# Performance work log

Measured on AMD Instinct MI355X. Metric: run time of the kernel, lower is better.

## Reference

```python
import jax, jax.numpy as jnp
import numpy as np

N = 100000
E = 1600000
IN_C, HID_C, OUT_C = 128, 128, 64


def setup_inputs() -> dict:
    key = jax.random.key(0)
    k_x, k_e, k_w1, k_w2 = jax.random.split(key, 4)
    x = jax.random.normal(k_x, (N, IN_C), dtype=jnp.float32)
    edge_index = jax.random.randint(k_e, (2, E), 0, N, dtype=jnp.int32)
    # nn.Linear default init: U(-1/sqrt(fan_in), 1/sqrt(fan_in)); bias init zeros per module
    lim1 = 1.0 / np.sqrt(IN_C)
    lim2 = 1.0 / np.sqrt(HID_C)
    W1 = jax.random.uniform(k_w1, (IN_C, HID_C), minval=-lim1, maxval=lim1, dtype=jnp.float32)
    b1 = jnp.zeros((HID_C,), dtype=jnp.float32)
    W2 = jax.random.uniform(k_w2, (HID_C, OUT_C), minval=-lim2, maxval=lim2, dtype=jnp.float32)
    b2 = jnp.zeros((OUT_C,), dtype=jnp.float32)
    return {"x": x, "edge_index": edge_index, "W1": W1, "b1": b1, "W2": W2, "b2": b2}


def _out_degree_gcn_conv(x, src, dst, W, b, n_nodes):
    # linear projection (no bias in lin)
    h = x @ W  # [N, out_c]
    # out-degree of each source node
    deg = jax.ops.segment_sum(jnp.ones((src.shape[0],), dtype=h.dtype), src, num_segments=n_nodes)
    deg_inv = 1.0 / jnp.maximum(deg, 1.0)  # clamp(min=1)
    h = h * deg_inv[:, None]
    # message: x_j = h[src]; aggregate: sum at dst
    out = jax.ops.segment_sum(h[src], dst, num_segments=n_nodes)  # [N, out_c]
    return out + b


def reference(x, edge_index, W1, b1, W2, b2):
    src, dst = edge_index[0], edge_index[1]
    n = x.shape[0]
    h = _out_degree_gcn_conv(x, src, dst, W1, b1, n)
    h = jax.nn.relu(h)
    # dropout p=0.0 -> identity
    out = _out_degree_gcn_conv(h, src, dst, W2, b2, n)
    return out
```

## Files before the change

### kernel.cpp

```cpp
#include <hip/hip_runtime.h>
#include <hip/hip_bf16.h>


typedef __attribute__((ext_vector_type(8))) short short8;
typedef __attribute__((ext_vector_type(4))) float floatx4;

__device__ inline unsigned short f2bf(float f) {
    union { float f; unsigned u; } v; v.f = f;
    return (unsigned short)((v.u + 0x8000u) >> 16);
}
__device__ inline float bf2f(unsigned b) {
    union { unsigned u; float f; } v; v.u = b << 16;
    return v.f;
}
__device__ inline float bf2f_hi(unsigned b) {
    union { unsigned u; float f; } v; v.u = b & 0xFFFF0000u;
    return v.f;
}

#define NBMAX 512
#define CAP   8192
#define CHUNK 8192

__global__ __launch_bounds__(256) void convw_kernel(
    const float* __restrict__ W1, const float* __restrict__ W2,
    unsigned short* __restrict__ Wb1, unsigned short* __restrict__ Wb2,
    int* __restrict__ cnt)
{
    int i = blockIdx.x * 256 + threadIdx.x;
    if (i < NBMAX * 32) cnt[i] = 0;
    if (i < 128 * 128) {
        int k = i >> 7, n = i & 127;
        Wb1[n * 128 + k] = f2bf(W1[k * 128 + n]);
    }
    i -= 128 * 128;
    if (i >= 0 && i < 128 * 64) {
        int k = i >> 6, n = i & 63;
        Wb2[n * 128 + k] = f2bf(W2[k * 64 + n]);
    }
}

#define SCAN512(lb, t)                                    \
    for (int o = 1; o < 512; o <<= 1) {                   \
        int add_ = ((t) >= o) ? lb[(t) - o] : 0;          \
        __syncthreads();                                  \
        lb[t] += add_;                                    \
        __syncthreads();                                  \
    }

__global__ __launch_bounds__(512) void scatter2_kernel(
    const int* __restrict__ src, const int* __restrict__ dst, int E,
    int* __restrict__ cnt_d, int* __restrict__ cnt_s,
    unsigned* __restrict__ pairs, unsigned char* __restrict__ srcs_b, int NB,
    const float* __restrict__ x, unsigned short* __restrict__ xb, int NF8)
{
    const int EB = (E + CHUNK - 1) / CHUNK;
    if ((int)blockIdx.x >= EB) {
        int i = ((int)blockIdx.x - EB) * 512 + threadIdx.x;
        if (i < NF8) {
            float4 a0 = ((const float4*)x)[(size_t)i * 2];
            float4 a1 = ((const float4*)x)[(size_t)i * 2 + 1];
            uint4 st;
            st.x = (unsigned)f2bf(a0.x) | ((unsigned)f2bf(a0.y) << 16);
            st.y = (unsigned)f2bf(a0.z) | ((unsigned)f2bf(a0.w) << 16);
            st.z = (unsigned)f2bf(a1.x) | ((unsigned)f2bf(a1.y) << 16);
            st.w = (unsigned)f2bf(a1.z) | ((unsigned)f2bf(a1.w) << 16);
            ((uint4*)xb)[i] = st;
        }
        return;
    }
    __shared__ int hd[NBMAX], lb[512], bd[NBMAX], cd_[NBMAX];
    __shared__ unsigned staged[CHUNK];
    const int t = threadIdx.x;
    const int e0 = blockIdx.x * CHUNK;
    const int e1 = min(e0 + CHUNK, E);
    const int cnt = e1 - e0;

    for (int i = t; i < NB; i += 512) { hd[i] = 0; cd_[i] = 0; }
    __syncthreads();
    for (int i = e0 + t; i < e1; i += 512)
        atomicAdd(&hd[dst[i] >> 8], 1);
    __syncthreads();
    lb[t] = (t < NB) ? hd[t] : 0;
    __syncthreads();
    SCAN512(lb, t)
    for (int i = t; i < NB; i += 512)
        if (hd[i]) bd[i] = atomicAdd(&cnt_d[i * 16], hd[i]);
    __syncthreads();
    for (int i = e0 + t; i < e1; i += 512) {
        int sv = src[i], dv = dst[i];
        int b = dv >> 8;
        int slot = atomicAdd(&cd_[b], 1);
        staged[lb[b] - hd[b] + slot] = ((unsigned)(dv & 255) << 24) | (unsigned)sv;
    }
    __syncthreads();
    for (int i = t; i < cnt; i += 512) {
        int lo = 0, hi = NB - 1;
        while (lo < hi) { int mid = (lo + hi) >> 1; if (lb[mid] > i) hi = mid; else lo = mid + 1; }
        int b = lo;
        pairs[(size_t)b * CAP + bd[b] + (i - (lb[b] - hd[b]))] = staged[i];
    }
    __syncthreads();

    unsigned char* stb = (unsigned char*)staged;
    for (int i = t; i < NB; i += 512) { hd[i] = 0; cd_[i] = 0; }
    __syncthreads();
    for (int i = e0 + t; i < e1; i += 512)
        atomicAdd(&hd[src[i] >> 8], 1);
    __syncthreads();
    lb[t] = (t < NB) ? hd[t] : 0;
    __syncthreads();
    SCAN512(lb, t)
    for (int i = t; i < NB; i += 512)
        if (hd[i]) bd[i] = atomicAdd(&cnt_s[i * 16], hd[i]);
    __syncthreads();
    for (int i = e0 + t; i < e1; i += 512) {
        int sv = src[i];
        int b = sv >> 8;
        int slot = atomicAdd(&cd_[b], 1);
        stb[lb[b] - hd[b] + slot] = (unsigned char)(sv & 255);
    }
    __syncthreads();
    for (int i = t; i < cnt; i += 512) {
        int lo = 0, hi = NB - 1;
        while (lo < hi) { int mid = (lo + hi) >> 1; if (lb[mid] > i) hi = mid; else lo = mid + 1; }
        int b = lo;
        srcs_b[(size_t)b * CAP + bd[b] + (i - (lb[b] - hd[b]))] = stb[i];
    }
}

__global__ __launch_bounds__(256) void bucket_finalize_kernel(
    const unsigned* __restrict__ pairs, const unsigned char* __restrict__ srcs_b,
    const int* __restrict__ cnt_d, const int* __restrict__ cnt_s,
    int* __restrict__ sorted_src, int2* __restrict__ se,
    float* __restrict__ deg_inv, int N)
{
    const int b = blockIdx.x;
    const int node0 = b << 8;
    const int t = threadIdx.x;
    const size_t base = (size_t)b * CAP;
    __shared__ int hist[256];
    __shared__ int cur[256];
    __shared__ int pre[256];

    const int cd = cnt_d[b * 16];
    hist[t] = 0;
    __syncthreads();
    for (int i = t; i < cd; i += 256)
        atomicAdd(&hist[pairs[base + i] >> 24], 1);
    __syncthreads();
    int v = hist[t];
    int v4 = (v + 3) & ~3;
    pre[t] = v4;
    __syncthreads();
    for (int o = 1; o < 256; o <<= 1) {
        int add = (t >= o) ? pre[t - o] : 0;
        __syncthreads();
        pre[t] += add;
        __syncthreads();
    }
    int excl = pre[t] - v4;
    cur[t] = excl;
    if (node0 + t < N) {
        se[node0 + t] = make_int2((int)base + excl, (int)base + excl + v);
        for (int i = v; i < v4; ++i) sorted_src[base + excl + i] = N;
    }
    __syncthreads();
    for (int i = t; i < cd; i += 256) {
        unsigned p = pairs[base + i];
        int pos = atomicAdd(&cur[p >> 24], 1);
        sorted_src[base + pos] = (int)(p & 0xFFFFFFu);
    }

    __syncthreads();
    hist[t] = 0;
    __syncthreads();
    const int cs = cnt_s[b * 16];
    for (int i = t; i < cs; i += 256)
        atomicAdd(&hist[srcs_b[base + i]], 1);
    __syncthreads();
    if (node0 + t < N) {
        int d = hist[t];
        deg_inv[node0 + t] = 1.0f / (float)(d < 1 ? 1 : d);
    }
}

template <int NC, int SC>
__global__ __launch_bounds__(256) void gemm_mfma_kernel(
    const unsigned short* __restrict__ Ab, const unsigned short* __restrict__ Wb,
    const float* __restrict__ scale, unsigned short* __restrict__ Cb, int M)
{
    constexpr int NT = NC / 16;
    const int t = threadIdx.x;
    if (blockIdx.x == 0 && t < NC / 2)
        ((unsigned*)Cb)[(size_t)M * (NC / 2) + t] = 0;
    const int wm = t >> 6;
    const int lane = t & 63;
    const int lm = lane & 15;
    const int lk = (lane >> 4) * 8;

    const int r0 = blockIdx.x * 64 + wm * 16;
    int row = r0 + lm;
    if (row >= M) row = M - 1;

    floatx4 acc[NT];
#pragma unroll
    for (int j = 0; j < NT; ++j) acc[j] = (floatx4){0.f, 0.f, 0.f, 0.f};

#pragma unroll
    for (int kk = 0; kk < 4; ++kk) {
        const int kb = kk * 32 + lk;
        short8 af = *(const short8*)&Ab[(size_t)row * 128 + kb];
#pragma unroll
        for (int j = 0; j < NT; ++j) {
            short8 bfr = *(const short8*)&Wb[(size_t)(j * 16 + lm) * 128 + kb];
            acc[j] = __builtin_amdgcn_mfma_f32_16x16x32_bf16(af, bfr, acc[j], 0, 0, 0);
        }
    }

    const int rbase = r0 + (lane >> 4) * 4;
#pragma unroll
    for (int reg = 0; reg < 4; ++reg) {
        int rg = rbase + reg;
        if (rg < M) {
            float di = SC ? scale[rg] : 1.0f;
#pragma unroll
            for (int j = 0; j < NT; ++j)
                Cb[(size_t)rg * NC + j * 16 + lm] = f2bf(SC ? acc[j][reg] * di : acc[j][reg]);
        }
    }
}

#define LD128(vv, ii) uint2 vv = *(const uint2*)&val[(size_t)(ii) * 64 + 2 * l]
#define ACC8_128(I0, I1) do { \
    LD128(v0, I0.x); LD128(v1, I0.y); LD128(v2, I0.z); LD128(v3, I0.w); \
    LD128(v4, I1.x); LD128(v5, I1.y); LD128(v6, I1.z); LD128(v7, I1.w); \
    a0 += ((bf2f(v0.x & 0xFFFF) + bf2f(v1.x & 0xFFFF)) + (bf2f(v2.x & 0xFFFF) + bf2f(v3.x & 0xFFFF))) \
        + ((bf2f(v4.x & 0xFFFF) + bf2f(v5.x & 0xFFFF)) + (bf2f(v6.x & 0xFFFF) + bf2f(v7.x & 0xFFFF))); \
    a1 += ((bf2f_hi(v0.x) + bf2f_hi(v1.x)) + (bf2f_hi(v2.x) + bf2f_hi(v3.x))) \
        + ((bf2f_hi(v4.x) + bf2f_hi(v5.x)) + (bf2f_hi(v6.x) + bf2f_hi(v7.x))); \
    a2 += ((bf2f(v0.y & 0xFFFF) + bf2f(v1.y & 0xFFFF)) + (bf2f(v2.y & 0xFFFF) + bf2f(v3.y & 0xFFFF))) \
        + ((bf2f(v4.y & 0xFFFF) + bf2f(v5.y & 0xFFFF)) + (bf2f(v6.y & 0xFFFF) + bf2f(v7.y & 0xFFFF))); \
    a3 += ((bf2f_hi(v0.y) + bf2f_hi(v1.y)) + (bf2f_hi(v2.y) + bf2f_hi(v3.y))) \
        + ((bf2f_hi(v4.y) + bf2f_hi(v5.y)) + (bf2f_hi(v6.y) + bf2f_hi(v7.y))); \
} while (0)
#define ACC4_128(I0) do { \
    LD128(v0, I0.x); LD128(v1, I0.y); LD128(v2, I0.z); LD128(v3, I0.w); \
    a0 += (bf2f(v0.x & 0xFFFF) + bf2f(v1.x & 0xFFFF)) + (bf2f(v2.x & 0xFFFF) + bf2f(v3.x & 0xFFFF)); \
    a1 += (bf2f_hi(v0.x) + bf2f_hi(v1.x)) + (bf2f_hi(v2.x) + bf2f_hi(v3.x)); \
    a2 += (bf2f(v0.y & 0xFFFF) + bf2f(v1.y & 0xFFFF)) + (bf2f(v2.y & 0xFFFF) + bf2f(v3.y & 0xFFFF)); \
    a3 += (bf2f_hi(v0.y) + bf2f_hi(v1.y)) + (bf2f_hi(v2.y) + bf2f_hi(v3.y)); \
} while (0)

__global__ __launch_bounds__(256) void aggregate128_kernel(
    const int2* __restrict__ se, const int* __restrict__ sorted_src,
    const unsigned* __restrict__ val, const float* __restrict__ bias,
    const float* __restrict__ deg_inv, unsigned* __restrict__ outb, int N)
{
    int node = blockIdx.x * 8 + (threadIdx.x >> 5);
    if (node >= N) return;
    int l = threadIdx.x & 31;
    int2 r = se[node];
    int e = r.x;
    const int end4 = r.x + ((r.y - r.x + 3) & ~3);
    float a0 = 0.f, a1 = 0.f, a2 = 0.f, a3 = 0.f;

    if (e + 8 <= end4) {
        int4 i0 = *(const int4*)&sorted_src[e];
        int4 i1 = *(const int4*)&sorted_src[e + 4];
        for (; e + 16 <= end4; e += 8) {
            int4 n0 = *(const int4*)&sorted_src[e + 8];
            int4 n1 = *(const int4*)&sorted_src[e + 12];
            ACC8_128(i0, i1);
            i0 = n0; i1 = n1;
        }
        ACC8_128(i0, i1);
        e += 8;
    }
    if (e < end4) {
        int4 i0 = *(const int4*)&sorted_src[e];
        ACC4_128(i0);
    }

    float di = deg_inv[node];
    float4 bv = *(const float4*)&bias[4 * l];
    a0 = fmaxf(a0 + bv.x, 0.f) * di;
    a1 = fmaxf(a1 + bv.y, 0.f) * di;
    a2 = fmaxf(a2 + bv.z, 0.f) * di;
    a3 = fmaxf(a3 + bv.w, 0.f) * di;
    uint2 o;
    o.x = (unsigned)f2bf(a0) | ((unsigned)f2bf(a1) << 16);
    o.y = (unsigned)f2bf(a2) | ((unsigned)f2bf(a3) << 16);
    *(uint2*)&outb[(size_t)node * 64 + 2 * l] = o;
}

#define LD64(vv, ii) unsigned vv = val[(size_t)(ii) * 32 + l]
#define ACC8_64(I0, I1) do { \
    LD64(v0, I0.x); LD64(v1, I0.y); LD64(v2, I0.z); LD64(v3, I0.w); \
    LD64(v4, I1.x); LD64(v5, I1.y); LD64(v6, I1.z); LD64(v7, I1.w); \
    ax += ((bf2f(v0 & 0xFFFF) + bf2f(v1 & 0xFFFF)) + (bf2f(v2 & 0xFFFF) + bf2f(v3 & 0xFFFF))) \
        + ((bf2f(v4 & 0xFFFF) + bf2f(v5 & 0xFFFF)) + (bf2f(v6 & 0xFFFF) + bf2f(v7 & 0xFFFF))); \
    ay += ((bf2f_hi(v0) + bf2f_hi(v1)) + (bf2f_hi(v2) + bf2f_hi(v3))) \
        + ((bf2f_hi(v4) + bf2f_hi(v5)) + (bf2f_hi(v6) + bf2f_hi(v7))); \
} while (0)
#define ACC4_64(I0) do { \
    LD64(v0, I0.x); LD64(v1, I0.y); LD64(v2, I0.z); LD64(v3, I0.w); \
    ax += (bf2f(v0 & 0xFFFF) + bf2f(v1 & 0xFFFF)) + (bf2f(v2 & 0xFFFF) + bf2f(v3 & 0xFFFF)); \
    ay += (bf2f_hi(v0) + bf2f_hi(v1)) + (bf2f_hi(v2) + bf2f_hi(v3)); \
} while (0)

__global__ __launch_bounds__(256) void aggregate64_kernel(
    const int2* __restrict__ se, const int* __restrict__ sorted_src,
    const unsigned* __restrict__ val, const float* __restrict__ bias,
    float* __restrict__ out, int N)
{
    int node = blockIdx.x * 8 + (threadIdx.x >> 5);
    if (node >= N) return;
    int l = threadIdx.x & 31;
    int2 r = se[node];
    int e = r.x;
    const int end4 = r.x + ((r.y - r.x + 3) & ~3);
    float ax = 0.f, ay = 0.f;

    if (e + 8 <= end4) {
        int4 i0 = *(const int4*)&sorted_src[e];
        int4 i1 = *(const int4*)&sorted_src[e + 4];
        for (; e + 16 <= end4; e += 8) {
            int4 n0 = *(const int4*)&sorted_src[e + 8];
            int4 n1 = *(const int4*)&sorted_src[e + 12];
            ACC8_64(i0, i1);
            i0 = n0; i1 = n1;
        }
        ACC8_64(i0, i1);
        e += 8;
    }
    if (e < end4) {
        int4 i0 = *(const int4*)&sorted_src[e];
        ACC4_64(i0);
    }

    float2 o = make_float2(ax + bias[2 * l], ay + bias[2 * l + 1]);
    *(float2*)&out[(size_t)node * 64 + 2 * l] = o;
}

extern "C" void kernel_launch(void* const* d_in, const int* in_sizes, int n_in,
                              void* d_out, int out_size, void* d_ws, size_t ws_size,
                              hipStream_t stream) {
    const float* x  = (const float*)d_in[0];
    const int*   ei = (const int*)d_in[1];
    const float* W1 = (const float*)d_in[2];
    const float* b1 = (const float*)d_in[3];
    const float* W2 = (const float*)d_in[4];
    const float* b2 = (const float*)d_in[5];
    float* out = (float*)d_out;

    const int N = in_sizes[0] / 128;
    const int E = in_sizes[1] / 2;
    const int* src = ei;
    const int* dst = ei + E;
    const int NB = (N + 255) >> 8;

    char* ws = (char*)d_ws;
    size_t off = 0;
    auto alloc = [&](size_t bytes) {
        void* p = ws + off;
        off = (off + bytes + 255) & ~(size_t)255;
        return p;
    };
    float* deg_inv  = (float*)alloc((size_t)N * 4);
    int2*  se       = (int2*)alloc((size_t)N * 8);
    int*   cnt_d    = (int*)alloc((size_t)NBMAX * 16 * 4 * 2);
    int*   cnt_s    = cnt_d + (size_t)NBMAX * 16;
    unsigned short* Wb1 = (unsigned short*)alloc((size_t)128 * 128 * 2);
    unsigned short* Wb2 = (unsigned short*)alloc((size_t)64 * 128 * 2);
    unsigned*      pairs  = (unsigned*)alloc((size_t)NBMAX * CAP * 4);
    unsigned char* srcs_b = (unsigned char*)alloc((size_t)NBMAX * CAP);
    int*   sorted_src = (int*)alloc((size_t)NBMAX * CAP * 4);
    unsigned short* h    = (unsigned short*)alloc((size_t)(N + 1) * 128 * 2);
    unsigned short* out1 = (unsigned short*)alloc((size_t)N * 128 * 2);
    unsigned short* xb = out1;
    unsigned short* g = ((size_t)(N + 1) * 128 <= (size_t)NBMAX * CAP * 4)
                            ? (unsigned short*)pairs
                            : (unsigned short*)alloc((size_t)(N + 1) * 64 * 2);

    convw_kernel<<<96, 256, 0, stream>>>(W1, W2, Wb1, Wb2, cnt_d);

    const int EB = (E + CHUNK - 1) / CHUNK;
    const int NF8 = (N * 128) / 8;
    const int CB = (NF8 + 511) / 512;
    scatter2_kernel<<<EB + CB, 512, 0, stream>>>(src, dst, E, cnt_d, cnt_s,
                                                 pairs, srcs_b, NB, x, xb, NF8);
    bucket_finalize_kernel<<<NB, 256, 0, stream>>>(pairs, srcs_b, cnt_d, cnt_s,
                                                   sorted_src, se, deg_inv, N);

    const int gblocks = (N + 63) / 64;
    const int ablocks = (N + 7) / 8;
    gemm_mfma_kernel<128, 1><<<gblocks, 256, 0, stream>>>(xb, Wb1, deg_inv, h, N);
    aggregate128_kernel<<<ablocks, 256, 0, stream>>>(se, sorted_src, (const unsigned*)h, b1,
                                                     deg_inv, (unsigned*)out1, N);
    gemm_mfma_kernel<64, 0><<<gblocks, 256, 0, stream>>>(out1, Wb2, nullptr, g, N);
    aggregate64_kernel<<<ablocks, 256, 0, stream>>>(se, sorted_src, (const unsigned*)g, b2, out, N);
}
```

Measured before the change: 306.8 us.

## Split scatter into per-key blocks, widen blocks, use warp-per-bucket copyout

The scatter kernel now launches separate blocks for the dst-bucketing and src-bucketing phases instead of running both sequentially in one block, and block size goes from 512 to 1024 threads. The per-element binary search for the global copyout is replaced by one wavefront per bucket copying contiguous runs. bucket_finalize goes from 256 to 512 threads. The aim is more parallelism and cheaper, coalesced writes in the preprocessing stage, at the cost of more blocks, more barriers and heavier per-block LDS use.

```diff
diff --git a/kernel.cpp b/kernel.cpp
--- a/kernel.cpp
+++ b/kernel.cpp
@@ -40,23 +40,17 @@
     }
 }
 
-#define SCAN512(lb, t)                                    \
-    for (int o = 1; o < 512; o <<= 1) {                   \
-        int add_ = ((t) >= o) ? lb[(t) - o] : 0;          \
-        __syncthreads();                                  \
-        lb[t] += add_;                                    \
-        __syncthreads();                                  \
-    }
-
-__global__ __launch_bounds__(512) void scatter2_kernel(
+__global__ __launch_bounds__(1024) void scatter2_kernel(
     const int* __restrict__ src, const int* __restrict__ dst, int E,
     int* __restrict__ cnt_d, int* __restrict__ cnt_s,
     unsigned* __restrict__ pairs, unsigned char* __restrict__ srcs_b, int NB,
     const float* __restrict__ x, unsigned short* __restrict__ xb, int NF8)
 {
     const int EB = (E + CHUNK - 1) / CHUNK;
-    if ((int)blockIdx.x >= EB) {
-        int i = ((int)blockIdx.x - EB) * 512 + threadIdx.x;
+    const int t = threadIdx.x;
+    const int bid = blockIdx.x;
+    if (bid >= 2 * EB) {
+        int i = (bid - 2 * EB) * 1024 + t;
         if (i < NF8) {
             float4 a0 = ((const float4*)x)[(size_t)i * 2];
             float4 a1 = ((const float4*)x)[(size_t)i * 2 + 1];
@@ -69,67 +63,70 @@
         }
         return;
     }
-    __shared__ int hd[NBMAX], lb[512], bd[NBMAX], cd_[NBMAX];
+    __shared__ int hd[NBMAX], lb[NBMAX], bd[NBMAX], cd_[NBMAX];
     __shared__ unsigned staged[CHUNK];
-    const int t = threadIdx.x;
-    const int e0 = blockIdx.x * CHUNK;
+    const bool phaseA = (bid < EB);
+    const int c = phaseA ? bid : bid - EB;
+    const int e0 = c * CHUNK;
     const int e1 = min(e0 + CHUNK, E);
-    const int cnt = e1 - e0;
-
-    for (int i = t; i < NB; i += 512) { hd[i] = 0; cd_[i] = 0; }
-    __syncthreads();
-    for (int i = e0 + t; i < e1; i += 512)
-        atomicAdd(&hd[dst[i] >> 8], 1);
-    __syncthreads();
-    lb[t] = (t < NB) ? hd[t] : 0;
-    __syncthreads();
-    SCAN512(lb, t)
-    for (int i = t; i < NB; i += 512)
-        if (hd[i]) bd[i] = atomicAdd(&cnt_d[i * 16], hd[i]);
-    __syncthreads();
-    for (int i = e0 + t; i < e1; i += 512) {
-        int sv = src[i], dv = dst[i];
-        int b = dv >> 8;
-        int slot = atomicAdd(&cd_[b], 1);
-        staged[lb[b] - hd[b] + slot] = ((unsigned)(dv & 255) << 24) | (unsigned)sv;
-    }
-    __syncthreads();
-    for (int i = t; i < cnt; i += 512) {
-        int lo = 0, hi = NB - 1;
-        while (lo < hi) { int mid = (lo + hi) >> 1; if (lb[mid] > i) hi = mid; else lo = mid + 1; }
-        int b = lo;
-        pairs[(size_t)b * CAP + bd[b] + (i - (lb[b] - hd[b]))] = staged[i];
-    }
-    __syncthreads();
-
-    unsigned char* stb = (unsigned char*)staged;
-    for (int i = t; i < NB; i += 512) { hd[i] = 0; cd_[i] = 0; }
-    __syncthreads();
-    for (int i = e0 + t; i < e1; i += 512)
-        atomicAdd(&hd[src[i] >> 8], 1);
-    __syncthreads();
-    lb[t] = (t < NB) ? hd[t] : 0;
-    __syncthreads();
-    SCAN512(lb, t)
-    for (int i = t; i < NB; i += 512)
-        if (hd[i]) bd[i] = atomicAdd(&cnt_s[i * 16], hd[i]);
-    __syncthreads();
-    for (int i = e0 + t; i < e1; i += 512) {
-        int sv = src[i];
-        int b = sv >> 8;
-        int slot = atomicAdd(&cd_[b], 1);
-        stb[lb[b] - hd[b] + slot] = (unsigned char)(sv & 255);
-    }
-    __syncthreads();
-    for (int i = t; i < cnt; i += 512) {
-        int lo = 0, hi = NB - 1;
-        while (lo < hi) { int mid = (lo + hi) >> 1; if (lb[mid] > i) hi = mid; else lo = mid + 1; }
-        int b = lo;
-        srcs_b[(size_t)b * CAP + bd[b] + (i - (lb[b] - hd[b]))] = stb[i];
-    }
-}
-
-__global__ __launch_bounds__(256) void bucket_finalize_kernel(
+    const int* __restrict__ key = phaseA ? dst : src;
+
+    for (int i = t; i < NB; i += 1024) { hd[i] = 0; cd_[i] = 0; }
+    __syncthreads();
+    for (int i = e0 + t; i < e1; i += 1024)
+        atomicAdd(&hd[key[i] >> 8], 1);
+    __syncthreads();
+    if (t < NBMAX) lb[t] = (t < NB) ? hd[t] : 0;
+    __syncthreads();
+    for (int o = 1; o < NBMAX; o <<= 1) {
+        int add = (t >= o && t < NBMAX) ? lb[t - o] : 0;
+        __syncthreads();
+        if (t < NBMAX) lb[t] += add;
+        __syncthreads();
+    }
+    int* __restrict__ gcnt = phaseA ? cnt_d : cnt_s;
+    for (int i = t; i < NB; i += 1024)
+        if (hd[i]) bd[i] = atomicAdd(&gcnt[i * 16], hd[i]);
+    __syncthreads();
+
+    const int wid = t >> 6, lane = t & 63;
+    if (phaseA) {
+        for (int i = e0 + t; i < e1; i += 1024) {
+            int sv = src[i], dv = dst[i];
+            int b = dv >> 8;
+            int slot = atomicAdd(&cd_[b], 1);
+            staged[lb[b] - hd[b] + slot] = ((unsigned)(dv & 255) << 24) | (unsigned)sv;
+        }
+        __syncthreads();
+        for (int b = wid; b < NB; b += 16) {
+            int len = hd[b];
+            if (!len) continue;
+            int start = lb[b] - len;
+            size_t gbase = (size_t)b * CAP + bd[b];
+            for (int j = lane; j < len; j += 64)
+                pairs[gbase + j] = staged[start + j];
+        }
+    } else {
+        unsigned char* stb = (unsigned char*)staged;
+        for (int i = e0 + t; i < e1; i += 1024) {
+            int sv = src[i];
+            int b = sv >> 8;
+            int slot = atomicAdd(&cd_[b], 1);
+            stb[lb[b] - hd[b] + slot] = (unsigned char)(sv & 255);
+        }
+        __syncthreads();
+        for (int b = wid; b < NB; b += 16) {
+            int len = hd[b];
+            if (!len) continue;
+            int start = lb[b] - len;
+            size_t gbase = (size_t)b * CAP + bd[b];
+            for (int j = lane; j < len; j += 64)
+                srcs_b[gbase + j] = stb[start + j];
+        }
+    }
+}
+
+__global__ __launch_bounds__(512) void bucket_finalize_kernel(
     const unsigned* __restrict__ pairs, const unsigned char* __restrict__ srcs_b,
     const int* __restrict__ cnt_d, const int* __restrict__ cnt_s,
     int* __restrict__ sorted_src, int2* __restrict__ se,
@@ -144,42 +141,47 @@
     __shared__ int pre[256];
 
     const int cd = cnt_d[b * 16];
-    hist[t] = 0;
-    __syncthreads();
-    for (int i = t; i < cd; i += 256)
+    if (t < 256) hist[t] = 0;
+    __syncthreads();
+    for (int i = t; i < cd; i += 512)
         atomicAdd(&hist[pairs[base + i] >> 24], 1);
     __syncthreads();
-    int v = hist[t];
-    int v4 = (v + 3) & ~3;
-    pre[t] = v4;
+    int v = 0, v4 = 0;
+    if (t < 256) {
+        v = hist[t];
+        v4 = (v + 3) & ~3;
+        pre[t] = v4;
+    }
     __syncthreads();
     for (int o = 1; o < 256; o <<= 1) {
-        int add = (t >= o) ? pre[t - o] : 0;
-        __syncthreads();
-        pre[t] += add;
-        __syncthreads();
-    }
-    int excl = pre[t] - v4;
-    cur[t] = excl;
-    if (node0 + t < N) {
-        se[node0 + t] = make_int2((int)base + excl, (int)base + excl + v);
-        for (int i = v; i < v4; ++i) sorted_src[base + excl + i] = N;
-    }
-    __syncthreads();
-    for (int i = t; i < cd; i += 256) {
+        int add = (t >= o && t < 256) ? pre[t - o] : 0;
+        __syncthreads();
+        if (t < 256) pre[t] += add;
+        __syncthreads();
+    }
+    if (t < 256) {
+        int excl = pre[t] - v4;
+        cur[t] = excl;
+        if (node0 + t < N) {
+            se[node0 + t] = make_int2((int)base + excl, (int)base + excl + v);
+            for (int i = v; i < v4; ++i) sorted_src[base + excl + i] = N;
+        }
+    }
+    __syncthreads();
+    for (int i = t; i < cd; i += 512) {
         unsigned p = pairs[base + i];
         int pos = atomicAdd(&cur[p >> 24], 1);
         sorted_src[base + pos] = (int)(p & 0xFFFFFFu);
     }
 
     __syncthreads();
-    hist[t] = 0;
+    if (t < 256) hist[t] = 0;
     __syncthreads();
     const int cs = cnt_s[b * 16];
-    for (int i = t; i < cs; i += 256)
+    for (int i = t; i < cs; i += 512)
         atomicAdd(&hist[srcs_b[base + i]], 1);
     __syncthreads();
-    if (node0 + t < N) {
+    if (t < 256 && node0 + t < N) {
         int d = hist[t];
         deg_inv[node0 + t] = 1.0f / (float)(d < 1 ? 1 : d);
     }
@@ -387,10 +389,10 @@
 
     const int EB = (E + CHUNK - 1) / CHUNK;
     const int NF8 = (N * 128) / 8;
-    const int CB = (NF8 + 511) / 512;
-    scatter2_kernel<<<EB + CB, 512, 0, stream>>>(src, dst, E, cnt_d, cnt_s,
-                                                 pairs, srcs_b, NB, x, xb, NF8);
-    bucket_finalize_kernel<<<NB, 256, 0, stream>>>(pairs, srcs_b, cnt_d, cnt_s,
+    const int CB = (NF8 + 1023) / 1024;
+    scatter2_kernel<<<2 * EB + CB, 1024, 0, stream>>>(src, dst, E, cnt_d, cnt_s,
+                                                      pairs, srcs_b, NB, x, xb, NF8);
+    bucket_finalize_kernel<<<NB, 512, 0, stream>>>(pairs, srcs_b, cnt_d, cnt_s,
                                                    sorted_src, se, deg_inv, N);
 
     const int gblocks = (N + 63) / 64;
```

Result: faster. 277.8 us (-9.5%).
